# Kernel tuning notes

Hardware: AMD Instinct MI355X
Metric: run time of the kernel (lower is better)

Reference implementation:

```python
import jax, jax.numpy as jnp
import numpy as np

B, S, D, H = 4, 2048, 1024, 16
HD = D // H
NEG = -1e30


def setup_inputs() -> dict:
    key = jax.random.key(0)
    ks = jax.random.split(key, 6)
    scale = 1.0 / np.sqrt(D)
    return {
        "q": jax.random.normal(ks[0], (B, S, D), jnp.float32),
        "k": jax.random.normal(ks[1], (B, S, D), jnp.float32),
        "v": jax.random.normal(ks[2], (B, S, D), jnp.float32),
        "mask": jnp.ones((B, 1, S), jnp.float32),
        "wq": jax.random.normal(ks[3], (D, D), jnp.float32) * scale,
        "bq": jnp.zeros((D,), jnp.float32),
        "wk": jax.random.normal(ks[4], (D, D), jnp.float32) * scale,
        "bk": jnp.zeros((D,), jnp.float32),
        "wv": jax.random.normal(ks[5], (D, D), jnp.float32) * scale,
        "bv": jnp.zeros((D,), jnp.float32),
    }


def _heads(x):
    # (B,S,D) -> (B,H,S,HD)
    return x.reshape(B, S, H, HD).transpose(0, 2, 1, 3)


def reference(q, k, v, mask, wq, bq, wk, bk, wv, bv):
    # pointwise Conv1D(kernel=1) == linear: x @ W^T + b (W: (out,in))
    qh = _heads(jnp.einsum('bsd,ed->bse', q, wq) + bq)
    kh = _heads(jnp.einsum('bsd,ed->bse', k, wk) + bk)
    vh = _heads(jnp.einsum('bsd,ed->bse', v, wv) + bv)
    scores = jnp.einsum('bhqd,bhkd->bhqk', qh, kh) / jnp.sqrt(jnp.float32(HD))
    # mask_logits: x + (1 - mask) * -1e30, mask (B,1,S) -> (B,1,1,S)
    scores = scores + (1.0 - mask[:, None, :, :]) * NEG
    probs = jax.nn.softmax(scores, axis=-1)  # dropout is identity in eval
    ctx = jnp.einsum('bhqk,bhkd->bhqd', probs, vh)
    return ctx.transpose(0, 2, 1, 3).reshape(B, S, D)
```

## Files before the change

kernel.cpp:

```cpp
#include <hip/hip_runtime.h>
#include <math.h>

typedef __attribute__((ext_vector_type(8)))  _Float16 f16x8;
typedef __attribute__((ext_vector_type(4)))  _Float16 f16x4;
typedef __attribute__((ext_vector_type(2)))  __fp16   h16x2;
typedef __attribute__((ext_vector_type(4)))  float    f32x4;
typedef __attribute__((ext_vector_type(16))) float    f32x16;
typedef unsigned int u32;

static constexpr int B  = 4;
static constexpr int S  = 2048;
static constexpr int D  = 1024;
static constexpr int H  = 16;
static constexpr int HD = 64;

union U64cvt { f16x4 h; ushort4 u; };
union W4 { u32 w[4]; f16x8 v; };

__device__ __forceinline__ void gld16(const void* g, void* l) {
    __builtin_amdgcn_global_load_lds((const u32*)g, (u32*)l, 16, 0, 0);
}

__device__ __forceinline__ void cvtwr16(const float4& x, const float4& y, void* dst) {
    W4 w;
    w.w[0] = __builtin_bit_cast(u32, __builtin_amdgcn_cvt_pkrtz(x.x, x.y));
    w.w[1] = __builtin_bit_cast(u32, __builtin_amdgcn_cvt_pkrtz(x.z, x.w));
    w.w[2] = __builtin_bit_cast(u32, __builtin_amdgcn_cvt_pkrtz(y.x, y.y));
    w.w[3] = __builtin_bit_cast(u32, __builtin_amdgcn_cvt_pkrtz(y.z, y.w));
    *(f16x8*)dst = w.v;
}

__global__ __launch_bounds__(256)
void cvt_prep(const float* __restrict__ q, const float* __restrict__ k,
              const float* __restrict__ v,
              const float* __restrict__ wq, const float* __restrict__ wk,
              const float* __restrict__ wv,
              unsigned short* __restrict__ dst)
{
    const int c = blockIdx.x * 256 + threadIdx.x;
    const float* src;
    size_t idx;
    if (c < 3145728) {
        const int a = c >> 20;
        src = (a == 0) ? q : (a == 1) ? k : v;
        idx = (size_t)(c & 1048575) * 8;
    } else {
        const int c2 = c - 3145728;
        const int a = c2 >> 17;
        src = (a == 0) ? wq : (a == 1) ? wk : wv;
        idx = (size_t)(c2 & 131071) * 8;
    }
    const float4 x = *(const float4*)(src + idx);
    const float4 y = *(const float4*)(src + idx + 4);
    cvtwr16(x, y, dst + (size_t)c * 8);
}

__global__ __launch_bounds__(256)
void proj_f16(const unsigned short* __restrict__ af16,
              const unsigned short* __restrict__ wf16,
              const float* __restrict__ bqp, const float* __restrict__ bkp,
              const float* __restrict__ bvp,
              unsigned short* __restrict__ outs)
{
    const int bid = blockIdx.x;
    const int xcd = bid & 7;
    const int idx = bid >> 3;
    const int z   = idx / 64;
    const int r2  = idx - z * 64;
    const int mpl = r2 >> 3;
    const int np  = r2 & 7;
    const int mp  = (xcd >> 1) * 16 + (xcd & 1) * 8 + mpl;
    const int m0  = mp * 128;
    const int n0  = np * 128;

    const unsigned short* A  = af16 + (size_t)z * 8388608;
    const unsigned short* Wf = wf16 + (size_t)z * 1048576;
    const float* bias = (z == 0) ? bqp : (z == 1) ? bkp : bvp;
    unsigned short* out = outs + (size_t)z * 8388608;

    const int tid  = threadIdx.x;
    const int lane = tid & 63;
    const int wid  = tid >> 6;
    const int wr   = wid >> 1;
    const int wc   = wid & 1;

    __shared__ __align__(16) unsigned char lA[2][8192];
    __shared__ __align__(16) unsigned char lB[2][8192];

    f32x4 acc[4][4];
#pragma unroll
    for (int i = 0; i < 4; ++i)
#pragma unroll
        for (int j = 0; j < 4; ++j) acc[i][j] = (f32x4){0.f, 0.f, 0.f, 0.f};

    int grow[2], gcol[2], lbase[2];
#pragma unroll
    for (int i = 0; i < 2; ++i) {
        const int c = tid + 256 * i;
        grow[i]  = c >> 2;
        gcol[i]  = ((c & 3) - (grow[i] >> 1)) & 3;
        lbase[i] = (c & ~63) * 16;
    }

#pragma unroll
    for (int i = 0; i < 2; ++i) {
        gld16(A  + (size_t)(m0 + grow[i]) * D + gcol[i] * 8, lA[0] + lbase[i]);
        gld16(Wf + (size_t)(n0 + grow[i]) * D + gcol[i] * 8, lB[0] + lbase[i]);
    }
    __syncthreads();

    for (int kt = 0; kt < 32; ++kt) {
        const int cb = kt & 1, nx = cb ^ 1;

        if (kt < 31) {
            const int k1 = (kt + 1) * 32;
#pragma unroll
            for (int i = 0; i < 2; ++i) {
                gld16(A  + (size_t)(m0 + grow[i]) * D + k1 + gcol[i] * 8, lA[nx] + lbase[i]);
                gld16(Wf + (size_t)(n0 + grow[i]) * D + k1 + gcol[i] * 8, lB[nx] + lbase[i]);
            }
        }

        f16x8 af[4], bf[4];
#pragma unroll
        for (int mi = 0; mi < 4; ++mi) {
            const int row = wr * 64 + mi * 16 + (lane & 15);
            const int cc  = ((lane >> 4) + (row >> 1)) & 3;
            af[mi] = *(const f16x8*)(lA[cb] + row * 64 + cc * 16);
        }
#pragma unroll
        for (int ni = 0; ni < 4; ++ni) {
            const int row = wc * 64 + ni * 16 + (lane & 15);
            const int cc  = ((lane >> 4) + (row >> 1)) & 3;
            bf[ni] = *(const f16x8*)(lB[cb] + row * 64 + cc * 16);
        }

        __builtin_amdgcn_s_setprio(1);
#pragma unroll
        for (int mi = 0; mi < 4; ++mi)
#pragma unroll
            for (int ni = 0; ni < 4; ++ni)
                acc[mi][ni] = __builtin_amdgcn_mfma_f32_16x16x32_f16(af[mi], bf[ni], acc[mi][ni], 0, 0, 0);
        __builtin_amdgcn_s_setprio(0);

        __syncthreads();
    }

#pragma unroll
    for (int mi = 0; mi < 4; ++mi) {
        const int gmBase = m0 + wr * 64 + mi * 16 + ((lane >> 4) << 2);
        const int b  = gmBase >> 11;
        const int s0 = gmBase & 2047;
        const int tV   = s0 >> 6;
        const int kv6  = s0 & 63;
        const int ksg  = kv6 >> 4;
        const int hi2v = (kv6 >> 3) & 1;
        const int jb   = kv6 & 7;
#pragma unroll
        for (int ni = 0; ni < 4; ++ni) {
            const int gn = n0 + wc * 64 + ni * 16 + (lane & 15);
            const float bb = bias[gn];
            const int hh = gn >> 6;
            const int hd = gn & 63;
            const size_t bhbase = ((size_t)b * H + hh) * ((size_t)S * HD);
            if (z == 0) {
#pragma unroll
                for (int r = 0; r < 4; ++r) {
                    const int gm = gmBase + r;
                    const _Float16 hv = (_Float16)(acc[mi][ni][r] + bb);
                    out[bhbase + (size_t)(gm & 2047) * HD + hd] =
                        __builtin_bit_cast(unsigned short, hv);
                }
            } else if (z == 1) {
                const int ks   = hd >> 4;
                const int hi2k = (hd >> 3) & 1;
                const int j    = hd & 7;
#pragma unroll
                for (int r = 0; r < 4; ++r) {
                    const int s = (gmBase + r) & 2047;
                    const int t = s >> 6;
                    const int q = ((s >> 5) & 1) * 4 + ks;
                    const _Float16 hv = (_Float16)(acc[mi][ni][r] + bb);
                    out[bhbase + (((size_t)t * 8 + q) * 64 + hi2k * 32 + (s & 31)) * 8 + j] =
                        __builtin_bit_cast(unsigned short, hv);
                }
            } else {
                const int nb  = hd >> 5;
                const int c31 = hd & 31;
                const int q   = nb * 4 + ksg;
                U64cvt uu;
#pragma unroll
                for (int r = 0; r < 4; ++r)
                    uu.h[r] = (_Float16)(acc[mi][ni][r] + bb);
                *(ushort4*)(out + bhbase +
                    (((size_t)tV * 8 + q) * 64 + hi2v * 32 + c31) * 8 + jb) = uu.u;
            }
        }
    }
}

__global__ __launch_bounds__(256)
void proj_qkv(const float* __restrict__ qi, const float* __restrict__ ki,
              const float* __restrict__ vi,
              const float* __restrict__ wqp, const float* __restrict__ wkp,
              const float* __restrict__ wvp,
              const float* __restrict__ bqp, const float* __restrict__ bkp,
              const float* __restrict__ bvp,
              unsigned short* __restrict__ ws)
{
    const int bid = blockIdx.x;
    const int xcd = bid & 7;
    const int idx = bid >> 3;
    const int z   = idx / 64;
    const int r2  = idx - z * 64;
    const int mpl = r2 >> 3;
    const int np  = r2 & 7;
    const int mp  = (xcd >> 1) * 16 + (xcd & 1) * 8 + mpl;
    const int m0  = mp * 128;
    const int n0  = np * 128;

    const float* A    = (z == 0) ? qi  : (z == 1) ? ki  : vi;
    const float* W    = (z == 0) ? wqp : (z == 1) ? wkp : wvp;
    const float* bias = (z == 0) ? bqp : (z == 1) ? bkp : bvp;
    unsigned short* out = ws + (size_t)z * ((size_t)B * S * D);

    const int tid  = threadIdx.x;
    const int lane = tid & 63;
    const int wid  = tid >> 6;
    const int wr   = wid >> 1;
    const int wc   = wid & 1;

    __shared__ __align__(16) unsigned char lA[2][8192];
    __shared__ __align__(16) unsigned char lB[2][8192];

    f32x4 acc[4][4];
#pragma unroll
    for (int i = 0; i < 4; ++i)
#pragma unroll
        for (int j = 0; j < 4; ++j) acc[i][j] = (f32x4){0.f, 0.f, 0.f, 0.f};

    const int rb = (lane >> 4) * 16;

    int srow[2], sc8[2], soff[2];
#pragma unroll
    for (int i = 0; i < 2; ++i) {
        const int f = tid + 256 * i;
        srow[i] = f >> 2;
        sc8[i]  = f & 3;
        soff[i] = ((f >> 2) * 64 + (f & 3) * 16) ^ ((((f >> 2)) & 7) << 4);
    }

#pragma unroll
    for (int i = 0; i < 2; ++i) {
        const float* pa = A + (size_t)(m0 + srow[i]) * D + sc8[i] * 8;
        const float* pw = W + (size_t)(n0 + srow[i]) * D + sc8[i] * 8;
        cvtwr16(*(const float4*)pa, *(const float4*)(pa + 4), lA[0] + soff[i]);
        cvtwr16(*(const float4*)pw, *(const float4*)(pw + 4), lB[0] + soff[i]);
    }
    float4 pa0[2], pa1[2], pw0[2], pw1[2];
#pragma unroll
    for (int i = 0; i < 2; ++i) {
        const float* pa = A + (size_t)(m0 + srow[i]) * D + 32 + sc8[i] * 8;
        const float* pw = W + (size_t)(n0 + srow[i]) * D + 32 + sc8[i] * 8;
        pa0[i] = *(const float4*)pa;  pa1[i] = *(const float4*)(pa + 4);
        pw0[i] = *(const float4*)pw;  pw1[i] = *(const float4*)(pw + 4);
    }
    __syncthreads();

    for (int kt = 0; kt < 32; ++kt) {
        const int cb = kt & 1, nx = cb ^ 1;
        if (kt < 31) {
#pragma unroll
            for (int i = 0; i < 2; ++i) {
                cvtwr16(pa0[i], pa1[i], lA[nx] + soff[i]);
                cvtwr16(pw0[i], pw1[i], lB[nx] + soff[i]);
            }
        }
        f16x8 af[4], bf[4];
#pragma unroll
        for (int mi = 0; mi < 4; ++mi) {
            const int row = wr * 64 + mi * 16 + (lane & 15);
            af[mi] = *(const f16x8*)(lA[cb] + ((row * 64 + rb) ^ ((row & 7) << 4)));
        }
#pragma unroll
        for (int ni = 0; ni < 4; ++ni) {
            const int row = wc * 64 + ni * 16 + (lane & 15);
            bf[ni] = *(const f16x8*)(lB[cb] + ((row * 64 + rb) ^ ((row & 7) << 4)));
        }
        if (kt < 30) {
            const int k2 = (kt + 2) * 32;
#pragma unroll
            for (int i = 0; i < 2; ++i) {
                const float* pa = A + (size_t)(m0 + srow[i]) * D + k2 + sc8[i] * 8;
                const float* pw = W + (size_t)(n0 + srow[i]) * D + k2 + sc8[i] * 8;
                pa0[i] = *(const float4*)pa;  pa1[i] = *(const float4*)(pa + 4);
                pw0[i] = *(const float4*)pw;  pw1[i] = *(const float4*)(pw + 4);
            }
        }
        __builtin_amdgcn_s_setprio(1);
#pragma unroll
        for (int mi = 0; mi < 4; ++mi)
#pragma unroll
            for (int ni = 0; ni < 4; ++ni)
                acc[mi][ni] = __builtin_amdgcn_mfma_f32_16x16x32_f16(af[mi], bf[ni], acc[mi][ni], 0, 0, 0);
        __builtin_amdgcn_s_setprio(0);
        __syncthreads();
    }

#pragma unroll
    for (int mi = 0; mi < 4; ++mi) {
        const int gmBase = m0 + wr * 64 + mi * 16 + ((lane >> 4) << 2);
        const int b  = gmBase >> 11;
        const int s0 = gmBase & 2047;
        const int tV   = s0 >> 6;
        const int kv6  = s0 & 63;
        const int ksg  = kv6 >> 4;
        const int hi2v = (kv6 >> 3) & 1;
        const int jb   = kv6 & 7;
#pragma unroll
        for (int ni = 0; ni < 4; ++ni) {
            const int gn = n0 + wc * 64 + ni * 16 + (lane & 15);
            const float bb = bias[gn];
            const int hh = gn >> 6;
            const int hd = gn & 63;
            const size_t bhbase = ((size_t)b * H + hh) * ((size_t)S * HD);
            if (z == 0) {
#pragma unroll
                for (int r = 0; r < 4; ++r) {
                    const int gm = gmBase + r;
                    const _Float16 hv = (_Float16)(acc[mi][ni][r] + bb);
                    out[bhbase + (size_t)(gm & 2047) * HD + hd] =
                        __builtin_bit_cast(unsigned short, hv);
                }
            } else if (z == 1) {
                const int ks   = hd >> 4;
                const int hi2k = (hd >> 3) & 1;
                const int j    = hd & 7;
#pragma unroll
                for (int r = 0; r < 4; ++r) {
                    const int s = (gmBase + r) & 2047;
                    const int t = s >> 6;
                    const int q = ((s >> 5) & 1) * 4 + ks;
                    const _Float16 hv = (_Float16)(acc[mi][ni][r] + bb);
                    out[bhbase + (((size_t)t * 8 + q) * 64 + hi2k * 32 + (s & 31)) * 8 + j] =
                        __builtin_bit_cast(unsigned short, hv);
                }
            } else {
                const int nb  = hd >> 5;
                const int c31 = hd & 31;
                const int q   = nb * 4 + ksg;
                U64cvt uu;
#pragma unroll
                for (int r = 0; r < 4; ++r)
                    uu.h[r] = (_Float16)(acc[mi][ni][r] + bb);
                *(ushort4*)(out + bhbase +
                    (((size_t)tV * 8 + q) * 64 + hi2v * 32 + c31) * 8 + jb) = uu.u;
            }
        }
    }
}

__global__ __launch_bounds__(256)
void attn_f16(const unsigned short* __restrict__ qh,
              const unsigned short* __restrict__ kf,
              const unsigned short* __restrict__ vf,
              const float* __restrict__ mask,
              float* __restrict__ out)
{
    const int flat = blockIdx.y * gridDim.x + blockIdx.x;
    const int sw   = (flat & 7) * 128 + (flat >> 3);
    const int bh   = sw >> 4;
    const int q0   = (sw & 15) * 128;

    const int b = bh >> 4;
    const int h = bh & 15;
    const unsigned short* Q  = qh + (size_t)bh * S * HD;
    const unsigned short* KF = kf + (size_t)bh * S * HD;
    const unsigned short* VF = vf + (size_t)bh * S * HD;

    const int tid  = threadIdx.x;
    const int lane = tid & 63;
    const int wid  = tid >> 6;
    const int l31  = lane & 31;
    const int hi2  = lane >> 5;

    __shared__ __align__(16) unsigned char Kl[2][8192];
    __shared__ __align__(16) unsigned char Vl[2][8192];
    __shared__ __align__(16) float maskb[2][64];

    const int ldsA = wid * 1024;
    const int ldsB = wid * 1024 + 4096;
    const int g0   = tid * 8;
    const int g1   = tid * 8 + 2048;

    const float C = 0.18033688011112042f;
    const float SHIFT = -5.770780163555854f;

    f16x8 aq[4];
    {
        const unsigned short* qrow = Q + (size_t)(q0 + wid * 32 + l31) * HD;
#pragma unroll
        for (int ks = 0; ks < 4; ++ks)
            aq[ks] = *(const f16x8*)(qrow + ks * 16 + hi2 * 8);
    }

    f32x16 accO[2], accL;
    accO[0] = (f32x16){};
    accO[1] = (f32x16){};
    accL    = (f32x16){};
    const f16x8 onesv = {(_Float16)1.f, (_Float16)1.f, (_Float16)1.f, (_Float16)1.f,
                         (_Float16)1.f, (_Float16)1.f, (_Float16)1.f, (_Float16)1.f};

    gld16(KF + g0, Kl[0] + ldsA);
    gld16(KF + g1, Kl[0] + ldsB);
    gld16(VF + g0, Vl[0] + ldsA);
    gld16(VF + g1, Vl[0] + ldsB);
    if (tid < 64)
        maskb[0][tid] = fmaf(1.0f - mask[(size_t)b * S + tid], -1.4426950408889634e30f, SHIFT);
    __syncthreads();

    const int lane16 = lane * 16;
    for (int t = 0; t < S / 64; ++t) {
        const int cb = t & 1, nx = cb ^ 1;
        const unsigned char* Kc = Kl[cb];
        const unsigned char* Vc = Vl[cb];

        if (t < S / 64 - 1) {
            const int nt = (t + 1) * 4096;
            gld16(KF + nt + g0, Kl[nx] + ldsA);
            gld16(KF + nt + g1, Kl[nx] + ldsB);
            gld16(VF + nt + g0, Vl[nx] + ldsA);
            gld16(VF + nt + g1, Vl[nx] + ldsB);
            if (tid < 64)
                maskb[nx][tid] = fmaf(1.0f - mask[(size_t)b * S + (t + 1) * 64 + tid],
                                      -1.4426950408889634e30f, SHIFT);
        }

        f32x16 p[2];
        p[0] = (f32x16){};
        p[1] = (f32x16){};
        __builtin_amdgcn_s_setprio(1);
#pragma unroll
        for (int kb = 0; kb < 2; ++kb)
#pragma unroll
            for (int ks = 0; ks < 4; ++ks) {
                const f16x8 ak = *(const f16x8*)(Kc + lane16 + (kb * 4 + ks) * 1024);
                p[kb] = __builtin_amdgcn_mfma_f32_32x32x16_f16(ak, aq[ks], p[kb], 0, 0, 0);
            }
        __builtin_amdgcn_s_setprio(0);

        f16x8 pa[4];
#pragma unroll
        for (int kb = 0; kb < 2; ++kb) {
            float pe[16];
#pragma unroll
            for (int g = 0; g < 4; ++g) {
                const f32x4 mg = *(const f32x4*)(&maskb[cb][kb * 32 + g * 8 + hi2 * 4]);
#pragma unroll
                for (int e = 0; e < 4; ++e)
                    pe[g * 4 + e] = exp2f(fmaf(p[kb][g * 4 + e], C, mg[e]));
            }
#pragma unroll
            for (int ks2 = 0; ks2 < 2; ++ks2) {
                const int o = ks2 * 8;
                u32 a0 = __builtin_bit_cast(u32, __builtin_amdgcn_cvt_pkrtz(pe[o + 0], pe[o + 1]));
                u32 a1 = __builtin_bit_cast(u32, __builtin_amdgcn_cvt_pkrtz(pe[o + 2], pe[o + 3]));
                u32 a2 = __builtin_bit_cast(u32, __builtin_amdgcn_cvt_pkrtz(pe[o + 4], pe[o + 5]));
                u32 a3 = __builtin_bit_cast(u32, __builtin_amdgcn_cvt_pkrtz(pe[o + 6], pe[o + 7]));
                asm volatile("v_permlane32_swap_b32 %0, %1" : "+v"(a0), "+v"(a2));
                asm volatile("v_permlane32_swap_b32 %0, %1" : "+v"(a1), "+v"(a3));
                W4 w;
                w.w[0] = a0; w.w[1] = a1; w.w[2] = a2; w.w[3] = a3;
                pa[kb * 2 + ks2] = w.v;
            }
        }

        __builtin_amdgcn_s_setprio(1);
#pragma unroll
        for (int nb = 0; nb < 2; ++nb)
#pragma unroll
            for (int ksg = 0; ksg < 4; ++ksg) {
                const f16x8 bv = *(const f16x8*)(Vc + lane16 + (nb * 4 + ksg) * 1024);
                accO[nb] = __builtin_amdgcn_mfma_f32_32x32x16_f16(pa[ksg], bv, accO[nb], 0, 0, 0);
            }
#pragma unroll
        for (int ksg = 0; ksg < 4; ++ksg)
            accL = __builtin_amdgcn_mfma_f32_32x32x16_f16(pa[ksg], onesv, accL, 0, 0, 0);
        __builtin_amdgcn_s_setprio(0);

        __syncthreads();
    }

    float lr[16];
#pragma unroll
    for (int r = 0; r < 16; ++r)
        lr[r] = 1.0f / accL[r];

#pragma unroll
    for (int nb = 0; nb < 2; ++nb) {
        const int dcol = h * HD + nb * 32 + l31;
#pragma unroll
        for (int r = 0; r < 16; ++r) {
            const int qrow = q0 + wid * 32 + (r & 3) + 8 * (r >> 2) + 4 * hi2;
            out[((size_t)b * S + qrow) * D + dcol] = accO[nb][r] * lr[r];
        }
    }
}

extern "C" void kernel_launch(void* const* d_in, const int* in_sizes, int n_in,
                              void* d_out, int out_size, void* d_ws, size_t ws_size,
                              hipStream_t stream)
{
    const float* q    = (const float*)d_in[0];
    const float* k    = (const float*)d_in[1];
    const float* v    = (const float*)d_in[2];
    const float* mask = (const float*)d_in[3];
    const float* wq   = (const float*)d_in[4];
    const float* bq   = (const float*)d_in[5];
    const float* wk   = (const float*)d_in[6];
    const float* bk   = (const float*)d_in[7];
    const float* wv   = (const float*)d_in[8];
    const float* bv   = (const float*)d_in[9];

    unsigned short* ws = (unsigned short*)d_ws;
    const size_t per  = (size_t)B * S * D;
    const size_t wsz  = 1048576;
    const size_t need = (3 * per + 3 * wsz + 3 * per) * 2;

    dim3 ga(S / 128, B * H);
    if (ws_size >= need) {
        unsigned short* af16 = ws;
        unsigned short* wf16 = ws + 3 * per;
        unsigned short* outs = ws + 3 * per + 3 * wsz;
        cvt_prep<<<13824, 256, 0, stream>>>(q, k, v, wq, wk, wv, af16);
        proj_f16<<<1536, 256, 0, stream>>>(af16, wf16, bq, bk, bv, outs);
        attn_f16<<<ga, 256, 0, stream>>>(outs, outs + per, outs + 2 * per, mask, (float*)d_out);
    } else {
        proj_qkv<<<1536, 256, 0, stream>>>(q, k, v, wq, wk, wv, bq, bk, bv, ws);
        attn_f16<<<ga, 256, 0, stream>>>(ws, ws + per, ws + 2 * per, mask, (float*)d_out);
    }
}
```

Baseline: 228.9 us.

## Triple-buffer K/V with one barrier per tile and fdot2 row sums

Measured after the change: 228.0 us. Within noise of the previous version (-0.4%).

```diff
diff --git a/kernel.cpp b/kernel.cpp
--- a/kernel.cpp
+++ b/kernel.cpp
@@ -384,9 +384,9 @@
     const int l31  = lane & 31;
     const int hi2  = lane >> 5;
 
-    __shared__ __align__(16) unsigned char Kl[2][8192];
-    __shared__ __align__(16) unsigned char Vl[2][8192];
-    __shared__ __align__(16) float maskb[2][64];
+    __shared__ __align__(16) unsigned char Kl[3][8192];
+    __shared__ __align__(16) unsigned char Vl[3][8192];
+    __shared__ __align__(16) float maskall[2048];
 
     const int ldsA = wid * 1024;
     const int ldsB = wid * 1024 + 4096;
@@ -404,37 +404,60 @@
             aq[ks] = *(const f16x8*)(qrow + ks * 16 + hi2 * 8);
     }
 
-    f32x16 accO[2], accL;
+    float ls0 = 0.f, ls1 = 0.f;
+    f32x16 accO[2];
     accO[0] = (f32x16){};
     accO[1] = (f32x16){};
-    accL    = (f32x16){};
-    const f16x8 onesv = {(_Float16)1.f, (_Float16)1.f, (_Float16)1.f, (_Float16)1.f,
-                         (_Float16)1.f, (_Float16)1.f, (_Float16)1.f, (_Float16)1.f};
-
+    const h16x2 one2 = {(__fp16)1.0f, (__fp16)1.0f};
+
+    {
+        const float* mrow = mask + (size_t)b * S + tid * 8;
+        const float4 mv0 = *(const float4*)mrow;
+        const float4 mv1 = *(const float4*)(mrow + 4);
+        f32x4 t0, t1;
+        t0[0] = fmaf(1.0f - mv0.x, -1.4426950408889634e30f, SHIFT);
+        t0[1] = fmaf(1.0f - mv0.y, -1.4426950408889634e30f, SHIFT);
+        t0[2] = fmaf(1.0f - mv0.z, -1.4426950408889634e30f, SHIFT);
+        t0[3] = fmaf(1.0f - mv0.w, -1.4426950408889634e30f, SHIFT);
+        t1[0] = fmaf(1.0f - mv1.x, -1.4426950408889634e30f, SHIFT);
+        t1[1] = fmaf(1.0f - mv1.y, -1.4426950408889634e30f, SHIFT);
+        t1[2] = fmaf(1.0f - mv1.z, -1.4426950408889634e30f, SHIFT);
+        t1[3] = fmaf(1.0f - mv1.w, -1.4426950408889634e30f, SHIFT);
+        *(f32x4*)(maskall + tid * 8)     = t0;
+        *(f32x4*)(maskall + tid * 8 + 4) = t1;
+    }
     gld16(KF + g0, Kl[0] + ldsA);
     gld16(KF + g1, Kl[0] + ldsB);
     gld16(VF + g0, Vl[0] + ldsA);
     gld16(VF + g1, Vl[0] + ldsB);
-    if (tid < 64)
-        maskb[0][tid] = fmaf(1.0f - mask[(size_t)b * S + tid], -1.4426950408889634e30f, SHIFT);
+    gld16(KF + 4096 + g0, Kl[1] + ldsA);
+    gld16(KF + 4096 + g1, Kl[1] + ldsB);
+    gld16(VF + 4096 + g0, Vl[1] + ldsA);
+    gld16(VF + 4096 + g1, Vl[1] + ldsB);
     __syncthreads();
 
     const int lane16 = lane * 16;
-    for (int t = 0; t < S / 64; ++t) {
-        const int cb = t & 1, nx = cb ^ 1;
-        const unsigned char* Kc = Kl[cb];
-        const unsigned char* Vc = Vl[cb];
-
-        if (t < S / 64 - 1) {
-            const int nt = (t + 1) * 4096;
-            gld16(KF + nt + g0, Kl[nx] + ldsA);
-            gld16(KF + nt + g1, Kl[nx] + ldsB);
-            gld16(VF + nt + g0, Vl[nx] + ldsA);
-            gld16(VF + nt + g1, Vl[nx] + ldsB);
-            if (tid < 64)
-                maskb[nx][tid] = fmaf(1.0f - mask[(size_t)b * S + (t + 1) * 64 + tid],
-                                      -1.4426950408889634e30f, SHIFT);
-        }
+    int bi = 0;
+    for (int t = 0; t < 32; ++t) {
+        if (t < 31) {
+            asm volatile("s_waitcnt vmcnt(4)" ::: "memory");
+        } else {
+            asm volatile("s_waitcnt vmcnt(0)" ::: "memory");
+        }
+        __builtin_amdgcn_s_barrier();
+        __builtin_amdgcn_sched_barrier(0);
+
+        if (t < 30) {
+            const int b2 = (bi >= 1) ? bi - 1 : bi + 2;
+            const size_t nt = (size_t)(t + 2) * 4096;
+            gld16(KF + nt + g0, Kl[b2] + ldsA);
+            gld16(KF + nt + g1, Kl[b2] + ldsB);
+            gld16(VF + nt + g0, Vl[b2] + ldsA);
+            gld16(VF + nt + g1, Vl[b2] + ldsB);
+        }
+
+        const unsigned char* Kc = Kl[bi];
+        const unsigned char* Vc = Vl[bi];
 
         f32x16 p[2];
         p[0] = (f32x16){};
@@ -449,13 +472,14 @@
             }
         __builtin_amdgcn_s_setprio(0);
 
+        const float* mt = maskall + t * 64;
         f16x8 pa[4];
 #pragma unroll
         for (int kb = 0; kb < 2; ++kb) {
             float pe[16];
 #pragma unroll
             for (int g = 0; g < 4; ++g) {
-                const f32x4 mg = *(const f32x4*)(&maskb[cb][kb * 32 + g * 8 + hi2 * 4]);
+                const f32x4 mg = *(const f32x4*)(mt + kb * 32 + g * 8 + hi2 * 4);
 #pragma unroll
                 for (int e = 0; e < 4; ++e)
                     pe[g * 4 + e] = exp2f(fmaf(p[kb][g * 4 + e], C, mg[e]));
@@ -463,10 +487,18 @@
 #pragma unroll
             for (int ks2 = 0; ks2 < 2; ++ks2) {
                 const int o = ks2 * 8;
-                u32 a0 = __builtin_bit_cast(u32, __builtin_amdgcn_cvt_pkrtz(pe[o + 0], pe[o + 1]));
-                u32 a1 = __builtin_bit_cast(u32, __builtin_amdgcn_cvt_pkrtz(pe[o + 2], pe[o + 3]));
-                u32 a2 = __builtin_bit_cast(u32, __builtin_amdgcn_cvt_pkrtz(pe[o + 4], pe[o + 5]));
-                u32 a3 = __builtin_bit_cast(u32, __builtin_amdgcn_cvt_pkrtz(pe[o + 6], pe[o + 7]));
+                const h16x2 h0 = __builtin_amdgcn_cvt_pkrtz(pe[o + 0], pe[o + 1]);
+                const h16x2 h1 = __builtin_amdgcn_cvt_pkrtz(pe[o + 2], pe[o + 3]);
+                const h16x2 h2 = __builtin_amdgcn_cvt_pkrtz(pe[o + 4], pe[o + 5]);
+                const h16x2 h3 = __builtin_amdgcn_cvt_pkrtz(pe[o + 6], pe[o + 7]);
+                ls0 = __builtin_amdgcn_fdot2(h0, one2, ls0, false);
+                ls1 = __builtin_amdgcn_fdot2(h1, one2, ls1, false);
+                ls0 = __builtin_amdgcn_fdot2(h2, one2, ls0, false);
+                ls1 = __builtin_amdgcn_fdot2(h3, one2, ls1, false);
+                u32 a0 = __builtin_bit_cast(u32, h0);
+                u32 a1 = __builtin_bit_cast(u32, h1);
+                u32 a2 = __builtin_bit_cast(u32, h2);
+                u32 a3 = __builtin_bit_cast(u32, h3);
                 asm volatile("v_permlane32_swap_b32 %0, %1" : "+v"(a0), "+v"(a2));
                 asm volatile("v_permlane32_swap_b32 %0, %1" : "+v"(a1), "+v"(a3));
                 W4 w;
@@ -483,18 +515,19 @@
                 const f16x8 bv = *(const f16x8*)(Vc + lane16 + (nb * 4 + ksg) * 1024);
                 accO[nb] = __builtin_amdgcn_mfma_f32_32x32x16_f16(pa[ksg], bv, accO[nb], 0, 0, 0);
             }
-#pragma unroll
-        for (int ksg = 0; ksg < 4; ++ksg)
-            accL = __builtin_amdgcn_mfma_f32_32x32x16_f16(pa[ksg], onesv, accL, 0, 0, 0);
         __builtin_amdgcn_s_setprio(0);
 
-        __syncthreads();
-    }
+        bi = (bi == 2) ? 0 : bi + 1;
+    }
+
+    float lsum = ls0 + ls1;
+    lsum += __shfl_xor(lsum, 32);
+    const float linv = 1.0f / lsum;
 
     float lr[16];
 #pragma unroll
     for (int r = 0; r < 16; ++r)
-        lr[r] = 1.0f / accL[r];
+        lr[r] = __shfl(linv, (r & 3) + 8 * (r >> 2) + 4 * hi2);
 
 #pragma unroll
     for (int nb = 0; nb < 2; ++nb) {
```
